# Kernel optimization log

Measured on AMD Instinct MI355X. Metric: run time of the kernel, lower is better.

## Reference

```python
import jax, jax.numpy as jnp
import numpy as np

B, D_MODEL, D_HEAD, H, A = 1024, 1024, 64, 16, 4
EPS = 1e-6  # fast_transformers recurrent linear attention denominator eps


def setup_inputs() -> dict:
    key = jax.random.key(0)
    ks = jax.random.split(key, 24)
    s = 0.02
    n = jax.random.normal
    u = jax.random.uniform
    decay_u = u(ks[17], (H, D_HEAD), minval=0.001, maxval=0.2)
    return {
        "query": n(ks[0], (B, D_MODEL), jnp.float32),
        "key": n(ks[1], (B, D_MODEL), jnp.float32),
        "value": n(ks[2], (B, D_MODEL), jnp.float32),
        "matrix": n(ks[3], (B, H, D_HEAD, D_HEAD), jnp.float32) * 0.02,
        "normalizer": u(ks[4], (B, H, D_HEAD), jnp.float32) + 0.5,
        "Wq": n(ks[5], (H, D_HEAD, D_MODEL), jnp.float32) * s,
        "bq": jnp.zeros((H, D_HEAD), jnp.float32),
        "Wk": n(ks[6], (H, D_HEAD, D_MODEL), jnp.float32) * s,
        "bk": jnp.zeros((H, D_HEAD), jnp.float32),
        "Wv": n(ks[7], (H, D_HEAD, D_MODEL), jnp.float32) * s,
        "bv": jnp.zeros((H, D_HEAD), jnp.float32),
        "Wo": n(ks[8], (H, D_MODEL, D_HEAD), jnp.float32) * s,
        "bo": jnp.zeros((H, D_MODEL), jnp.float32),
        "We": n(ks[9], (H, D_MODEL), jnp.float32) * s,
        "be": jnp.zeros((H,), jnp.float32),
        "Ww": n(ks[10], (H, D_HEAD), jnp.float32) * s,
        "bw": jnp.zeros((H,), jnp.float32),
        "decay_logits": -jnp.log(1.0 / decay_u - 1.0),
    }


def reference(query, key, value, matrix, normalizer,
              Wq, bq, Wk, bk, Wv, bv, Wo, bo, We, be, Ww, bw, decay_logits):
    # ---- expert (head) routing: top-k over softmax of router logits ----
    logits = jnp.einsum('bm,hm->bh', query, We) + be          # [B,H]
    probs = jax.nn.softmax(logits, axis=-1)
    top_p, top_i = jax.lax.top_k(probs, A)                    # [B,A]
    top_logits = jnp.take_along_axis(logits, top_i, axis=-1)  # [B,A]

    # ---- banked head projections (compute all heads, gather active) ----
    def proj(x, W, b):
        return jnp.einsum('bm,hdm->bhd', x, W) + b            # [B,H,d]
    idx3 = top_i[:, :, None]
    q = jnp.take_along_axis(proj(query, Wq, bq), idx3, axis=1)  # [B,A,d]
    k = jnp.take_along_axis(proj(key, Wk, bk), idx3, axis=1)    # [B,A,d]
    v = jnp.take_along_axis(proj(value, Wv, bv), idx3, axis=1)  # [B,A,d]

    # ---- gather per-head recurrent state ----
    bidx = jnp.arange(B)[:, None]
    S = matrix[bidx, top_i]       # [B,A,d,d]
    Z = normalizer[bidx, top_i]   # [B,A,d]

    # ---- recurrent linear attention step (elu+1 feature map) ----
    phi_q = jax.nn.elu(q) + 1.0
    phi_k = jax.nn.elu(k) + 1.0
    dS = jnp.einsum('bad,bae->bade', phi_k, v)                # [B,A,d,d]
    S_new = S + dS
    Z_new = Z + phi_k
    num = jnp.einsum('bad,bade->bae', phi_q, S_new)
    den = jnp.einsum('bad,bad->ba', phi_q, Z_new) + EPS
    out = num / den[..., None]                                # [B,A,d]

    # ---- write gate + per-head decayed state update ----
    write_logits = top_logits + jnp.einsum('bad,bad->ba', out + q, Ww[top_i]) + bw[top_i]
    wp = jax.nn.sigmoid(write_logits)                         # [B,A]
    decay = jax.nn.sigmoid(decay_logits)[top_i]               # [B,A,d]
    Z_out = Z * (1.0 - wp[..., None] * decay) + wp[..., None] * phi_k
    S_out = S * (1.0 - wp[..., None, None] * decay[..., None]) + wp[..., None, None] * dS

    # ---- scatter updated states back into the full banks ----
    matrix_new = matrix.at[bidx, top_i].set(S_out)
    normalizer_new = normalizer.at[bidx, top_i].set(Z_out)

    # ---- merge heads: probability-weighted banked output projection ----
    # sum_a p_a * (Wo[i_a] @ out_a + bo[i_a]) == Wo applied to scatter of p*out
    full = jnp.zeros((B, H, D_HEAD), out.dtype).at[bidx, top_i].add(out * top_p[..., None])
    merged = jnp.einsum('bhe,hme->bm', full, Wo) + jnp.einsum('ba,bam->bm', top_p, bo[top_i])
    return merged, matrix_new, normalizer_new
```

## Files before the change

### kernel.cpp

```cpp
#include <hip/hip_runtime.h>
#include <hip/hip_bf16.h>

#define NB 1024
#define DM 1024
#define DH 64
#define NH 16
#define NA 4
#define FEPS 1e-6f

typedef __attribute__((ext_vector_type(8))) short s16x8;
typedef __attribute__((ext_vector_type(4))) float f32x4;

__device__ __forceinline__ unsigned short f2bf(float f) {
    unsigned u = __builtin_bit_cast(unsigned, f);
    u += 0x7FFFu + ((u >> 16) & 1u);
    return (unsigned short)(u >> 16);
}
__device__ __forceinline__ unsigned pk2(float x, float y) {
    return (unsigned)f2bf(x) | ((unsigned)f2bf(y) << 16);
}

__global__ __launch_bounds__(256) void k_route(
    const float* __restrict__ query,
    const float* __restrict__ We,
    const float* __restrict__ be,
    int* __restrict__ cnt,
    int* __restrict__ topi,
    float* __restrict__ topp,
    float* __restrict__ topl,
    int* __restrict__ slot,
    int* __restrict__ rows)
{
    int b = blockIdx.x, t = threadIdx.x;
    __shared__ float qs[DM];
    __shared__ float lg[NH];
    __shared__ int   sti[NA];
    __shared__ float stp[NA], stl[NA];
    ((float4*)qs)[t] = ((const float4*)(query + (size_t)b*DM))[t];
    __syncthreads();
    int h = t >> 4, l = t & 15;
    const float* w = We + h*DM;
    float p = 0.f;
    for (int j = l; j < DM; j += 16) p += qs[j]*w[j];
    #pragma unroll
    for (int d = 8; d > 0; d >>= 1) p += __shfl_down(p, d, 16);
    if (l == 0) lg[h] = p + be[h];
    __syncthreads();
    if (t == 0) {
        float mx = lg[0];
        for (int i = 1; i < NH; i++) mx = fmaxf(mx, lg[i]);
        float s = 0.f, e[NH];
        for (int i = 0; i < NH; i++) { e[i] = expf(lg[i]-mx); s += e[i]; }
        float inv = 1.f/s;
        unsigned used = 0;
        for (int a = 0; a < NA; a++) {
            int bi = -1; float bv = -1e30f;
            for (int i = 0; i < NH; i++)
                if (!((used>>i)&1u) && lg[i] > bv) { bv = lg[i]; bi = i; }
            used |= 1u << bi;
            sti[a] = bi; stp[a] = e[bi]*inv; stl[a] = lg[bi];
        }
    }
    __syncthreads();
    if (t < NA) {
        int hh = sti[t];
        topi[b*NA+t] = hh; topp[b*NA+t] = stp[t]; topl[b*NA+t] = stl[t];
        int pos = atomicAdd(&cnt[hh], 1);
        rows[hh*NB + pos] = b*NA + t;
    }
    if (t < NH) {
        int sl = -1;
        #pragma unroll
        for (int a = 0; a < NA; a++) if (sti[a] == t) sl = a;
        slot[b*NH + t] = sl;
    }
}

__global__ __launch_bounds__(256) void k_proj(
    const float* __restrict__ Xq, const float* __restrict__ Xk, const float* __restrict__ Xv,
    const float* __restrict__ Wq, const float* __restrict__ Wk, const float* __restrict__ Wv,
    const float* __restrict__ bq, const float* __restrict__ bk, const float* __restrict__ bv,
    const int* __restrict__ cnt, const int* __restrict__ rows,
    float* __restrict__ qb, float* __restrict__ kb, float* __restrict__ vb)
{
    int h = blockIdx.x, c = blockIdx.y, pz = blockIdx.z;
    int n = cnt[h];
    int r0 = c*64;
    if (r0 >= n) return;
    int nr = min(64, n - r0);
    const float* X    = pz==0 ? Xq : (pz==1 ? Xk : Xv);
    const float* W    = (pz==0 ? Wq : (pz==1 ? Wk : Wv)) + (size_t)h*DH*DM;
    const float* bias = (pz==0 ? bq : (pz==1 ? bk : bv)) + h*DH;
    float* outp = pz==0 ? qb : (pz==1 ? kb : vb);

    __shared__ __align__(16) unsigned short Af[4*2*64*8];
    __shared__ __align__(16) unsigned short Bf[4*2*64*8];
    __shared__ int codes[64];
    int t = threadIdx.x;
    if (t < 64) codes[t] = rows[h*NB + r0 + min(t, nr-1)];
    __syncthreads();

    int lane = t & 63, wv = t >> 6;
    int lr = t >> 2;
    int ks = (t & 3) * 16;
    int sA = ks >> 5;
    int g0 = (ks >> 3) & 3;
    int grp = lr >> 4;
    int dst0 = ((grp*2 + sA)*64 + (lr & 15) + g0*16) * 8;
    int dst1 = ((grp*2 + sA)*64 + (lr & 15) + (g0+1)*16) * 8;
    const float* srcA = X + (size_t)(codes[lr] >> 2)*DM + ks;
    const float* srcB = W + (size_t)lr*DM + ks;

    f32x4 acc[4] = {};
    for (int kt = 0; kt < DM; kt += 64) {
        float4 a0 = ((const float4*)(srcA + kt))[0];
        float4 a1 = ((const float4*)(srcA + kt))[1];
        float4 a2 = ((const float4*)(srcA + kt))[2];
        float4 a3 = ((const float4*)(srcA + kt))[3];
        float4 b0 = ((const float4*)(srcB + kt))[0];
        float4 b1 = ((const float4*)(srcB + kt))[1];
        float4 b2 = ((const float4*)(srcB + kt))[2];
        float4 b3 = ((const float4*)(srcB + kt))[3];
        uint4 pA0 = { pk2(a0.x,a0.y), pk2(a0.z,a0.w), pk2(a1.x,a1.y), pk2(a1.z,a1.w) };
        uint4 pA1 = { pk2(a2.x,a2.y), pk2(a2.z,a2.w), pk2(a3.x,a3.y), pk2(a3.z,a3.w) };
        uint4 pB0 = { pk2(b0.x,b0.y), pk2(b0.z,b0.w), pk2(b1.x,b1.y), pk2(b1.z,b1.w) };
        uint4 pB1 = { pk2(b2.x,b2.y), pk2(b2.z,b2.w), pk2(b3.x,b3.y), pk2(b3.z,b3.w) };
        *(uint4*)(Af + dst0) = pA0;
        *(uint4*)(Af + dst1) = pA1;
        *(uint4*)(Bf + dst0) = pB0;
        *(uint4*)(Bf + dst1) = pB1;
        __syncthreads();
        #pragma unroll
        for (int s = 0; s < 2; s++) {
            s16x8 av = *(const s16x8*)(Af + ((wv*2 + s)*64 + lane)*8);
            #pragma unroll
            for (int mt = 0; mt < 4; mt++) {
                s16x8 bv = *(const s16x8*)(Bf + ((mt*2 + s)*64 + lane)*8);
                acc[mt] = __builtin_amdgcn_mfma_f32_16x16x32_bf16(av, bv, acc[mt], 0, 0, 0);
            }
        }
        __syncthreads();
    }

    int rbase = wv*16 + (lane >> 4)*4;
    #pragma unroll
    for (int reg = 0; reg < 4; reg++) {
        int r = rbase + reg;
        if (r < nr) {
            int code = codes[r];
            float* dst = outp + (size_t)code*DH;
            #pragma unroll
            for (int mt = 0; mt < 4; mt++) {
                int m = mt*16 + (lane & 15);
                dst[m] = acc[mt][reg] + bias[m];
            }
        }
    }
}

__global__ __launch_bounds__(256) void k_update(
    const float* __restrict__ matrix,
    const float* __restrict__ normalizer,
    const float* __restrict__ Ww, const float* __restrict__ bw,
    const float* __restrict__ dlog,
    const int* __restrict__ slot, const float* __restrict__ topl,
    const float* __restrict__ qb, const float* __restrict__ kb,
    const float* __restrict__ vb, float* __restrict__ ob,
    float* __restrict__ om, float* __restrict__ on)
{
    int bh = blockIdx.x, t = threadIdx.x;
    const float* S = matrix + (size_t)bh*(DH*DH);
    float* So = om + (size_t)bh*(DH*DH);
    int sl = slot[bh];
    if (sl < 0) {
        #pragma unroll
        for (int j = 0; j < 4; j++) {
            int i4 = t + 256*j;
            ((float4*)So)[i4] = ((const float4*)S)[i4];
        }
        if (t < DH)
            on[(size_t)bh*DH + t] = normalizer[(size_t)bh*DH + t];
        return;
    }
    int b = bh >> 4, h = bh & 15;
    int code = b*NA + sl;
    __shared__ float st[DH*DH];
    __shared__ float pq[DH], pk[DH], vv[DH], qv[DH], Zs[DH];
    __shared__ float part[256];
    __shared__ float fd[DH], gd[DH];
    __shared__ float scal[4];
    if (t < DH) {
        float qq = qb[code*DH + t]; qv[t] = qq;
        float kk = kb[code*DH + t];
        pq[t] = qq > 0.f ? qq + 1.f : expf(qq);
        pk[t] = kk > 0.f ? kk + 1.f : expf(kk);
        vv[t] = vb[code*DH + t];
        Zs[t] = normalizer[(size_t)bh*DH + t];
    }
    #pragma unroll
    for (int j = 0; j < 4; j++)
        ((float4*)st)[t + 256*j] = ((const float4*)S)[t + 256*j];
    __syncthreads();
    {
        int e = t & 63, dg = t >> 6;
        float s = 0.f;
        #pragma unroll
        for (int d = 0; d < 16; d++) s += pq[dg*16 + d] * st[(dg*16+d)*DH + e];
        part[t] = s;
    }
    if (t < 64) {
        float r1 = pq[t]*pk[t];
        float r2 = pq[t]*(Zs[t]+pk[t]);
        #pragma unroll
        for (int d = 32; d > 0; d >>= 1) {
            r1 += __shfl_down(r1, d, 64);
            r2 += __shfl_down(r2, d, 64);
        }
        if (t == 0) { scal[0] = r1; scal[1] = r2 + FEPS; }
    }
    __syncthreads();
    float pqk = scal[0], den = scal[1];
    if (t < 64) {
        float cs = part[t] + part[64+t] + part[128+t] + part[192+t];
        float o = (cs + pqk*vv[t]) / den;
        ob[code*DH + t] = o;
        float r3 = (o + qv[t]) * Ww[h*DH + t];
        #pragma unroll
        for (int d = 32; d > 0; d >>= 1) r3 += __shfl_down(r3, d, 64);
        if (t == 0) {
            float wl = topl[code] + r3 + bw[h];
            scal[2] = 1.f/(1.f + expf(-wl));
        }
    }
    __syncthreads();
    float wp = scal[2];
    if (t < 64) {
        float dec = 1.f/(1.f + expf(-dlog[h*DH + t]));
        float f1 = 1.f - wp*dec;
        fd[t] = f1;
        gd[t] = wp*pk[t];
        on[(size_t)bh*DH + t] = Zs[t]*f1 + wp*pk[t];
    }
    __syncthreads();
    #pragma unroll
    for (int j = 0; j < 4; j++) {
        int i4 = t + 256*j;
        int d = i4 >> 4, e0 = (i4 & 15)*4;
        float4 f = ((const float4*)st)[i4];
        float F = fd[d], G = gd[d];
        float4 u = { f.x*F + G*vv[e0],   f.y*F + G*vv[e0+1],
                     f.z*F + G*vv[e0+2], f.w*F + G*vv[e0+3] };
        ((float4*)So)[i4] = u;
    }
}

__global__ __launch_bounds__(256) void k_mergemm(
    const float* __restrict__ Wo,
    const int* __restrict__ cnt, const int* __restrict__ rows,
    const float* __restrict__ topp, const float* __restrict__ ob,
    float* __restrict__ contrib)
{
    int h = blockIdx.x, rt = blockIdx.y, mtile = blockIdx.z;
    int n = cnt[h];
    int r0 = rt*64;
    if (r0 >= n) return;
    int nr = min(64, n - r0);

    __shared__ __align__(16) unsigned short Af[4*2*64*8];
    __shared__ __align__(16) unsigned short Bf[4*2*64*8];
    __shared__ int codes[64];
    int t = threadIdx.x;
    if (t < 64) codes[t] = rows[h*NB + r0 + min(t, nr-1)];
    __syncthreads();

    int lane = t & 63, wv = t >> 6;
    int lr = t >> 2;
    int es = (t & 3) * 16;
    int sA = es >> 5;
    int g0 = (es >> 3) & 3;
    int grp = lr >> 4;
    int dst0 = ((grp*2 + sA)*64 + (lr & 15) + g0*16) * 8;
    int dst1 = ((grp*2 + sA)*64 + (lr & 15) + (g0+1)*16) * 8;

    {
        int codeA = codes[lr];
        float sc = topp[codeA];
        const float* srcA = ob + (size_t)codeA*DH + es;
        const float* srcB = Wo + (size_t)h*DM*DH + (size_t)(mtile*64 + lr)*DH + es;
        float4 a0 = ((const float4*)srcA)[0];
        float4 a1 = ((const float4*)srcA)[1];
        float4 a2 = ((const float4*)srcA)[2];
        float4 a3 = ((const float4*)srcA)[3];
        float4 b0 = ((const float4*)srcB)[0];
        float4 b1 = ((const float4*)srcB)[1];
        float4 b2 = ((const float4*)srcB)[2];
        float4 b3 = ((const float4*)srcB)[3];
        uint4 pA0 = { pk2(a0.x*sc,a0.y*sc), pk2(a0.z*sc,a0.w*sc),
                      pk2(a1.x*sc,a1.y*sc), pk2(a1.z*sc,a1.w*sc) };
        uint4 pA1 = { pk2(a2.x*sc,a2.y*sc), pk2(a2.z*sc,a2.w*sc),
                      pk2(a3.x*sc,a3.y*sc), pk2(a3.z*sc,a3.w*sc) };
        uint4 pB0 = { pk2(b0.x,b0.y), pk2(b0.z,b0.w), pk2(b1.x,b1.y), pk2(b1.z,b1.w) };
        uint4 pB1 = { pk2(b2.x,b2.y), pk2(b2.z,b2.w), pk2(b3.x,b3.y), pk2(b3.z,b3.w) };
        *(uint4*)(Af + dst0) = pA0;
        *(uint4*)(Af + dst1) = pA1;
        *(uint4*)(Bf + dst0) = pB0;
        *(uint4*)(Bf + dst1) = pB1;
    }
    __syncthreads();

    f32x4 acc[4] = {};
    #pragma unroll
    for (int s = 0; s < 2; s++) {
        s16x8 av = *(const s16x8*)(Af + ((wv*2 + s)*64 + lane)*8);
        #pragma unroll
        for (int mt = 0; mt < 4; mt++) {
            s16x8 bv = *(const s16x8*)(Bf + ((mt*2 + s)*64 + lane)*8);
            acc[mt] = __builtin_amdgcn_mfma_f32_16x16x32_bf16(av, bv, acc[mt], 0, 0, 0);
        }
    }

    int rbase = wv*16 + (lane >> 4)*4;
    int mbase = mtile*64 + (lane & 15);
    #pragma unroll
    for (int reg = 0; reg < 4; reg++) {
        int r = rbase + reg;
        if (r < nr) {
            float* dst = contrib + (size_t)codes[r]*DM + mbase;
            #pragma unroll
            for (int mt = 0; mt < 4; mt++)
                dst[mt*16] = acc[mt][reg];
        }
    }
}

__global__ __launch_bounds__(256) void k_finalize(
    const int* __restrict__ topi, const float* __restrict__ topp,
    const float* __restrict__ bo, const float* __restrict__ contrib,
    float* __restrict__ merged)
{
    int b = blockIdx.x, t = threadIdx.x;
    __shared__ float tp[NA];
    __shared__ int   hh[NA];
    if (t < NA) { tp[t] = topp[b*NA+t]; hh[t] = topi[b*NA+t]; }
    __syncthreads();
    float ax = 0.f, ay = 0.f, az = 0.f, aw = 0.f;
    #pragma unroll
    for (int a = 0; a < NA; a++) {
        float4 cv = ((const float4*)(contrib + (size_t)(b*NA + a)*DM))[t];
        float4 w  = ((const float4*)(bo + (size_t)hh[a]*DM))[t];
        float p = tp[a];
        ax += cv.x + p*w.x; ay += cv.y + p*w.y;
        az += cv.z + p*w.z; aw += cv.w + p*w.w;
    }
    float4 u = { ax, ay, az, aw };
    ((float4*)merged)[(size_t)b*(DM/4) + t] = u;
}

extern "C" void kernel_launch(void* const* d_in, const int* in_sizes, int n_in,
                              void* d_out, int out_size, void* d_ws, size_t ws_size,
                              hipStream_t stream)
{
    const float* query  = (const float*)d_in[0];
    const float* key    = (const float*)d_in[1];
    const float* value  = (const float*)d_in[2];
    const float* matrix = (const float*)d_in[3];
    const float* normal = (const float*)d_in[4];
    const float* Wq = (const float*)d_in[5];
    const float* bq = (const float*)d_in[6];
    const float* Wk = (const float*)d_in[7];
    const float* bk = (const float*)d_in[8];
    const float* Wv = (const float*)d_in[9];
    const float* bv = (const float*)d_in[10];
    const float* Wo = (const float*)d_in[11];
    const float* bo = (const float*)d_in[12];
    const float* We = (const float*)d_in[13];
    const float* be = (const float*)d_in[14];
    const float* Ww = (const float*)d_in[15];
    const float* bw = (const float*)d_in[16];
    const float* dlog = (const float*)d_in[17];

    float* ws = (float*)d_ws;
    int*   cnt  = (int*)ws;
    int*   topi = (int*)(ws + 16);
    float* topp = ws + 16 + 4096;
    float* topl = topp + 4096;
    int*   slot = (int*)(topl + 4096);
    int*   rows = slot + 16384;
    float* qb = (float*)(rows + 16384);
    float* kb = qb + 262144;
    float* vb = kb + 262144;
    float* ob = vb + 262144;
    float* contrib = ob + 262144;

    float* out_merged = (float*)d_out;
    float* out_matrix = out_merged + (size_t)NB*DM;
    float* out_norm   = out_matrix + (size_t)NB*NH*DH*DH;

    hipMemsetAsync(cnt, 0, 16*sizeof(int), stream);
    k_route<<<NB, 256, 0, stream>>>(query, We, be, cnt, topi, topp, topl, slot, rows);
    k_proj<<<dim3(NH, NB/64, 3), 256, 0, stream>>>(query, key, value, Wq, Wk, Wv,
                                                   bq, bk, bv, cnt, rows, qb, kb, vb);
    k_update<<<NB*NH, 256, 0, stream>>>(matrix, normal, Ww, bw, dlog, slot, topl,
                                        qb, kb, vb, ob, out_matrix, out_norm);
    k_mergemm<<<dim3(NH, NB/64, DM/64), 256, 0, stream>>>(Wo, cnt, rows, topp, ob,
                                                          contrib);
    k_finalize<<<NB, 256, 0, stream>>>(topi, topp, bo, contrib, out_merged);
}
```

Measured before the change: 572.8 us.

## Split state update into active-head scalar kernel and flat streaming apply kernel

Result: slower. 598.9 us (+4.6%).

```diff
diff --git a/kernel.cpp b/kernel.cpp
--- a/kernel.cpp
+++ b/kernel.cpp
@@ -28,7 +28,6 @@
     int* __restrict__ topi,
     float* __restrict__ topp,
     float* __restrict__ topl,
-    int* __restrict__ slot,
     int* __restrict__ rows)
 {
     int b = blockIdx.x, t = threadIdx.x;
@@ -67,12 +66,6 @@
         topi[b*NA+t] = hh; topp[b*NA+t] = stp[t]; topl[b*NA+t] = stl[t];
         int pos = atomicAdd(&cnt[hh], 1);
         rows[hh*NB + pos] = b*NA + t;
-    }
-    if (t < NH) {
-        int sl = -1;
-        #pragma unroll
-        for (int a = 0; a < NA; a++) if (sti[a] == t) sl = a;
-        slot[b*NH + t] = sl;
     }
 }
 
@@ -158,37 +151,26 @@
     }
 }
 
-__global__ __launch_bounds__(256) void k_update(
+__global__ __launch_bounds__(256) void k_scal(
     const float* __restrict__ matrix,
     const float* __restrict__ normalizer,
     const float* __restrict__ Ww, const float* __restrict__ bw,
     const float* __restrict__ dlog,
-    const int* __restrict__ slot, const float* __restrict__ topl,
+    const int* __restrict__ topi, const float* __restrict__ topl,
     const float* __restrict__ qb, const float* __restrict__ kb,
     const float* __restrict__ vb, float* __restrict__ ob,
-    float* __restrict__ om, float* __restrict__ on)
-{
-    int bh = blockIdx.x, t = threadIdx.x;
+    float* __restrict__ fd_tab, float* __restrict__ gd_tab,
+    float* __restrict__ vv_tab, float* __restrict__ on)
+{
+    int code = blockIdx.x, t = threadIdx.x;
+    int b = code >> 2;
+    int h = topi[code];
+    int bh = b*NH + h;
     const float* S = matrix + (size_t)bh*(DH*DH);
-    float* So = om + (size_t)bh*(DH*DH);
-    int sl = slot[bh];
-    if (sl < 0) {
-        #pragma unroll
-        for (int j = 0; j < 4; j++) {
-            int i4 = t + 256*j;
-            ((float4*)So)[i4] = ((const float4*)S)[i4];
-        }
-        if (t < DH)
-            on[(size_t)bh*DH + t] = normalizer[(size_t)bh*DH + t];
-        return;
-    }
-    int b = bh >> 4, h = bh & 15;
-    int code = b*NA + sl;
     __shared__ float st[DH*DH];
     __shared__ float pq[DH], pk[DH], vv[DH], qv[DH], Zs[DH];
     __shared__ float part[256];
-    __shared__ float fd[DH], gd[DH];
-    __shared__ float scal[4];
+    __shared__ float scal2[4];
     if (t < DH) {
         float qq = qb[code*DH + t]; qv[t] = qq;
         float kk = kb[code*DH + t];
@@ -216,10 +198,10 @@
             r1 += __shfl_down(r1, d, 64);
             r2 += __shfl_down(r2, d, 64);
         }
-        if (t == 0) { scal[0] = r1; scal[1] = r2 + FEPS; }
-    }
-    __syncthreads();
-    float pqk = scal[0], den = scal[1];
+        if (t == 0) { scal2[0] = r1; scal2[1] = r2 + FEPS; }
+    }
+    __syncthreads();
+    float pqk = scal2[0], den = scal2[1];
     if (t < 64) {
         float cs = part[t] + part[64+t] + part[128+t] + part[192+t];
         float o = (cs + pqk*vv[t]) / den;
@@ -229,28 +211,54 @@
         for (int d = 32; d > 0; d >>= 1) r3 += __shfl_down(r3, d, 64);
         if (t == 0) {
             float wl = topl[code] + r3 + bw[h];
-            scal[2] = 1.f/(1.f + expf(-wl));
-        }
-    }
-    __syncthreads();
-    float wp = scal[2];
+            scal2[2] = 1.f/(1.f + expf(-wl));
+        }
+    }
+    __syncthreads();
+    float wp = scal2[2];
     if (t < 64) {
         float dec = 1.f/(1.f + expf(-dlog[h*DH + t]));
         float f1 = 1.f - wp*dec;
-        fd[t] = f1;
-        gd[t] = wp*pk[t];
-        on[(size_t)bh*DH + t] = Zs[t]*f1 + wp*pk[t];
-    }
-    __syncthreads();
-    #pragma unroll
-    for (int j = 0; j < 4; j++) {
-        int i4 = t + 256*j;
-        int d = i4 >> 4, e0 = (i4 & 15)*4;
-        float4 f = ((const float4*)st)[i4];
-        float F = fd[d], G = gd[d];
-        float4 u = { f.x*F + G*vv[e0],   f.y*F + G*vv[e0+1],
-                     f.z*F + G*vv[e0+2], f.w*F + G*vv[e0+3] };
-        ((float4*)So)[i4] = u;
+        float g = wp*pk[t];
+        size_t o8 = (size_t)bh*DH + t;
+        fd_tab[o8] = f1;
+        gd_tab[o8] = g;
+        vv_tab[o8] = vv[t];
+        on[o8] = Zs[t]*f1 + g;
+    }
+}
+
+__global__ __launch_bounds__(256) void k_apply(
+    const float* __restrict__ matrix,
+    const float* __restrict__ normalizer,
+    const float* __restrict__ fd_tab, const float* __restrict__ gd_tab,
+    const float* __restrict__ vv_tab,
+    float* __restrict__ om, float* __restrict__ on)
+{
+    size_t tid = (size_t)blockIdx.x*256 + threadIdx.x;
+    size_t nth = (size_t)gridDim.x*256;
+    const size_t n4 = (size_t)NB*NH*DH/4;
+    for (size_t i = tid; i < n4; i += nth) {
+        float4 g4 = ((const float4*)gd_tab)[i];
+        if (g4.x == 0.f)
+            ((float4*)on)[i] = ((const float4*)normalizer)[i];
+    }
+    const size_t m4 = (size_t)NB*NH*DH*DH/4;
+    for (size_t i = tid; i < m4; i += nth) {
+        int bh = (int)(i >> 10);
+        int d  = (int)((i >> 4) & 63);
+        int e4 = (int)(i & 15);
+        float G = gd_tab[bh*DH + d];
+        float4 f = ((const float4*)matrix)[i];
+        float4 u;
+        if (G != 0.f) {
+            float F = fd_tab[bh*DH + d];
+            float4 v = ((const float4*)vv_tab)[bh*16 + e4];
+            u = { f.x*F + G*v.x, f.y*F + G*v.y, f.z*F + G*v.z, f.w*F + G*v.w };
+        } else {
+            u = f;
+        }
+        ((float4*)om)[i] = u;
     }
 }
 
@@ -384,24 +392,30 @@
     int*   topi = (int*)(ws + 16);
     float* topp = ws + 16 + 4096;
     float* topl = topp + 4096;
-    int*   slot = (int*)(topl + 4096);
-    int*   rows = slot + 16384;
+    int*   rows = (int*)(topl + 4096);
     float* qb = (float*)(rows + 16384);
     float* kb = qb + 262144;
     float* vb = kb + 262144;
     float* ob = vb + 262144;
     float* contrib = ob + 262144;
+    float* fd_tab = contrib + (size_t)NB*NA*DM;
+    float* gd_tab = fd_tab + (size_t)NB*NH*DH;
+    float* vv_tab = gd_tab + (size_t)NB*NH*DH;
 
     float* out_merged = (float*)d_out;
     float* out_matrix = out_merged + (size_t)NB*DM;
     float* out_norm   = out_matrix + (size_t)NB*NH*DH*DH;
 
     hipMemsetAsync(cnt, 0, 16*sizeof(int), stream);
-    k_route<<<NB, 256, 0, stream>>>(query, We, be, cnt, topi, topp, topl, slot, rows);
+    hipMemsetAsync(gd_tab, 0, (size_t)NB*NH*DH*sizeof(float), stream);
+    k_route<<<NB, 256, 0, stream>>>(query, We, be, cnt, topi, topp, topl, rows);
     k_proj<<<dim3(NH, NB/64, 3), 256, 0, stream>>>(query, key, value, Wq, Wk, Wv,
                                                    bq, bk, bv, cnt, rows, qb, kb, vb);
-    k_update<<<NB*NH, 256, 0, stream>>>(matrix, normal, Ww, bw, dlog, slot, topl,
-                                        qb, kb, vb, ob, out_matrix, out_norm);
+    k_scal<<<NB*NA, 256, 0, stream>>>(matrix, normal, Ww, bw, dlog, topi, topl,
+                                      qb, kb, vb, ob, fd_tab, gd_tab, vv_tab,
+                                      out_norm);
+    k_apply<<<2048, 256, 0, stream>>>(matrix, normal, fd_tab, gd_tab, vv_tab,
+                                      out_matrix, out_norm);
     k_mergemm<<<dim3(NH, NB/64, DM/64), 256, 0, stream>>>(Wo, cnt, rows, topp, ob,
                                                           contrib);
     k_finalize<<<NB, 256, 0, stream>>>(topi, topp, bo, contrib, out_merged);
```
